# Optimization experiments

Measured on AMD Instinct MI355X. Metric: run time of the kernel, lower is better.

## Reference

```python
import jax, jax.numpy as jnp
import numpy as np
import math

# B graphs of exactly NMAX nodes each
N, B, NMAX, E = 131072, 256, 512, 1048576
F_IN, C, H, HEADS, NUM_CLASSES = 128, 32, 64, 4, 2
K1 = 128  # ceil(avg_num_nodes * pooling_ratio) = ceil(512 * 0.25)
SCALE = math.sqrt(H)  # GMT MAB scales by sqrt(dim_V), not sqrt(head_dim)


def gcn_conv(x, W, b, src, dst, n):
    h = x @ W
    deg = jax.ops.segment_sum(jnp.ones(dst.shape[0], x.dtype), dst, num_segments=n) + 1.0
    dinv = jax.lax.rsqrt(deg)
    msg = h[src] * (dinv[src] * dinv[dst])[:, None]
    out = jax.ops.segment_sum(msg, dst, num_segments=n)
    out = out + h * (dinv * dinv)[:, None]  # self-loop term
    return out + b


def mab(Qin, K, V, addmask, Wq, bq, Wo, bo):
    # GMT multihead attention block (layer_norm=False)
    Q = Qin @ Wq + bq
    b_, nq, _ = Q.shape
    dh = H // HEADS
    q = Q.reshape(b_, nq, HEADS, dh)
    k = K.reshape(b_, K.shape[1], HEADS, dh)
    v = V.reshape(b_, K.shape[1], HEADS, dh)
    s = jnp.einsum('bqhd,bkhd->bhqk', q, k) / SCALE
    if addmask is not None:
        s = s + addmask[:, None, None, :]  # mask invalid keys
    A = jax.nn.softmax(s, axis=-1)
    o = jnp.einsum('bhqk,bkhd->bqhd', A, v).reshape(b_, nq, H)
    o = Q + o
    return o + jax.nn.relu(o @ Wo + bo)


def _forward(x0, conv1_W, conv1_b, conv2_W, conv2_b, conv3_W, conv3_b,
             pool_lin1_W, pool_lin1_b,
             pma1_S, pma1_Wq, pma1_bq, pma1_Wk, pma1_bk, pma1_Wv, pma1_bv, pma1_Wo, pma1_bo,
             sab_Wq, sab_bq, sab_Wk, sab_bk, sab_Wv, sab_bv, sab_Wo, sab_bo,
             pma2_S, pma2_Wq, pma2_bq, pma2_Wk, pma2_bk, pma2_Wv, pma2_bv, pma2_Wo, pma2_bo,
             pool_lin2_W, pool_lin2_b, lin1_W, lin1_b, lin2_W, lin2_b,
             edge_index, batch):
    src, dst = edge_index[0], edge_index[1]
    x1 = jax.nn.relu(gcn_conv(x0, conv1_W, conv1_b, src, dst, N))
    x2 = jax.nn.relu(gcn_conv(x1, conv2_W, conv2_b, src, dst, N))
    x3 = jax.nn.relu(gcn_conv(x2, conv3_W, conv3_b, src, dst, N))
    xc = jnp.concatenate([x1, x2, x3], axis=-1)         # [N, 96]
    xl = xc @ pool_lin1_W + pool_lin1_b                 # [N, H] (GMT lin1)

    # to_dense_batch bookkeeping (batch is sorted per graph)
    counts = jax.ops.segment_sum(jnp.ones(N, jnp.int32), batch, num_segments=B)
    starts = jnp.cumsum(counts) - counts
    pos = jnp.arange(N, dtype=jnp.int32) - starts[batch]
    valid = jnp.zeros((B, NMAX), bool).at[batch, pos].set(True)
    addmask = jnp.where(valid, 0.0, -1e9).astype(xl.dtype)

    def dense(h):
        return jnp.zeros((B, NMAX, h.shape[-1]), h.dtype).at[batch, pos].set(h)

    # GMPool_G: seed queries attend over GCNConv-transformed node features
    Kd = dense(gcn_conv(xl, pma1_Wk, pma1_bk, src, dst, N))
    Vd = dense(gcn_conv(xl, pma1_Wv, pma1_bv, src, dst, N))
    Q = jnp.broadcast_to(pma1_S[None], (B, K1, H))
    bx = mab(Q, Kd, Vd, addmask, pma1_Wq, pma1_bq, pma1_Wo, pma1_bo)

    # SelfAtt (mask=None after first pool)
    bx = mab(bx, bx @ sab_Wk + sab_bk, bx @ sab_Wv + sab_bv, None,
             sab_Wq, sab_bq, sab_Wo, sab_bo)

    # GMPool_I with single seed (last pool -> 1 output node per graph)
    Q2 = jnp.broadcast_to(pma2_S[None], (B, 1, H))
    bx = mab(Q2, bx @ pma2_Wk + pma2_bk, bx @ pma2_Wv + pma2_bv, None,
             pma2_Wq, pma2_bq, pma2_Wo, pma2_bo)

    g = bx[:, 0] @ pool_lin2_W + pool_lin2_b            # [B, 32] (GMT lin2)
    h1 = jax.nn.relu(g @ lin1_W + lin1_b)               # dropout identity in eval
    logits = h1 @ lin2_W + lin2_b
    return jax.nn.log_softmax(logits, axis=-1)


def setup_inputs() -> dict:
    key = jax.random.key(0)
    ks = iter(jax.random.split(key, 80))
    def Wm(fi, fo):
        return jax.random.normal(next(ks), (fi, fo), jnp.float32) / np.sqrt(fi)
    def bv(fo):
        return jax.random.normal(next(ks), (fo,), jnp.float32) * 0.01
    inp = {}
    inp['x0'] = jax.random.normal(next(ks), (N, F_IN), jnp.float32)
    g = jax.random.randint(next(ks), (E,), 0, B)
    so = jax.random.randint(next(ks), (E,), 0, NMAX)
    do = jax.random.randint(next(ks), (E,), 0, NMAX)
    inp['edge_index'] = jnp.stack([g * NMAX + so, g * NMAX + do]).astype(jnp.int32)
    inp['batch'] = jnp.arange(N, dtype=jnp.int32) // NMAX
    inp['conv1_W'], inp['conv1_b'] = Wm(F_IN, C), bv(C)
    inp['conv2_W'], inp['conv2_b'] = Wm(C, C), bv(C)
    inp['conv3_W'], inp['conv3_b'] = Wm(C, C), bv(C)
    inp['pool_lin1_W'], inp['pool_lin1_b'] = Wm(3 * C, H), bv(H)
    inp['pma1_S'] = jax.random.normal(next(ks), (K1, H), jnp.float32)
    for p in ['pma1', 'sab', 'pma2']:
        for nm in ['q', 'k', 'v', 'o']:
            inp[p + '_W' + nm], inp[p + '_b' + nm] = Wm(H, H), bv(H)
    inp['pma2_S'] = jax.random.normal(next(ks), (1, H), jnp.float32)
    inp['pool_lin2_W'], inp['pool_lin2_b'] = Wm(H, C), bv(C)
    inp['lin1_W'], inp['lin1_b'] = Wm(C, 16), bv(16)
    inp['lin2_W'], inp['lin2_b'] = Wm(16, NUM_CLASSES), bv(NUM_CLASSES)
    return inp


def reference(x0, edge_index, batch, conv1_W, conv1_b, conv2_W, conv2_b, conv3_W, conv3_b,
              pool_lin1_W, pool_lin1_b,
              pma1_S, pma1_Wq, pma1_bq, pma1_Wk, pma1_bk, pma1_Wv, pma1_bv, pma1_Wo, pma1_bo,
              sab_Wq, sab_bq, sab_Wk, sab_bk, sab_Wv, sab_bv, sab_Wo, sab_bo,
              pma2_S, pma2_Wq, pma2_bq, pma2_Wk, pma2_bk, pma2_Wv, pma2_bv, pma2_Wo, pma2_bo,
              pool_lin2_W, pool_lin2_b, lin1_W, lin1_b, lin2_W, lin2_b):
    return _forward(x0, conv1_W, conv1_b, conv2_W, conv2_b, conv3_W, conv3_b,
                    pool_lin1_W, pool_lin1_b,
                    pma1_S, pma1_Wq, pma1_bq, pma1_Wk, pma1_bk, pma1_Wv, pma1_bv, pma1_Wo, pma1_bo,
                    sab_Wq, sab_bq, sab_Wk, sab_bk, sab_Wv, sab_bv, sab_Wo, sab_bo,
                    pma2_S, pma2_Wq, pma2_bq, pma2_Wk, pma2_bk, pma2_Wv, pma2_bv, pma2_Wo, pma2_bo,
                    pool_lin2_W, pool_lin2_b, lin1_W, lin1_b, lin2_W, lin2_b,
                    edge_index, batch)
```

## Files before the change

kernel.cpp:

```cpp
#include <hip/hip_runtime.h>
#include <hip/hip_bf16.h>

#define N_NODES 131072
#define NGRAPH  256
#define NMAXN   512
#define NEDGE   1048576
#define FIN     128
#define HDIM    64
#define K1Q     128
#define EPB     1024
#define NBLK    (NEDGE / EPB)

__global__ __launch_bounds__(256) void k_hist2(const int* __restrict__ dst,
                                               int* __restrict__ h) {
    __shared__ int lh[NGRAPH];
    const int tid = threadIdx.x;
    lh[tid] = 0;
    __syncthreads();
    const int base = blockIdx.x * EPB;
#pragma unroll
    for (int j = 0; j < 4; ++j)
        atomicAdd(&lh[dst[base + j * 256 + tid] >> 9], 1);
    __syncthreads();
    h[blockIdx.x * 256 + tid] = lh[tid];
}

__global__ __launch_bounds__(256) void k_scan_bins(int* __restrict__ h,
                                                   int* __restrict__ binTot) {
    const int b = blockIdx.x;
    const int tid = threadIdx.x;
    int v[4], s = 0;
#pragma unroll
    for (int j = 0; j < 4; ++j) { v[j] = h[(tid * 4 + j) * 256 + b]; s += v[j]; }
    __shared__ int sc[256];
    sc[tid] = s;
    __syncthreads();
    for (int o = 1; o < 256; o <<= 1) {
        int t = (tid >= o) ? sc[tid - o] : 0;
        __syncthreads();
        sc[tid] += t;
        __syncthreads();
    }
    int run = sc[tid] - s;
#pragma unroll
    for (int j = 0; j < 4; ++j) { int t = v[j]; h[(tid * 4 + j) * 256 + b] = run; run += t; }
    if (tid == 255) binTot[b] = sc[255];
}

__global__ __launch_bounds__(256) void k_binstart(const int* __restrict__ binTot,
                                                  int* __restrict__ starts) {
    const int tid = threadIdx.x;
    int v = binTot[tid];
    __shared__ int sc[256];
    sc[tid] = v;
    __syncthreads();
    for (int o = 1; o < 256; o <<= 1) {
        int t = (tid >= o) ? sc[tid - o] : 0;
        __syncthreads();
        sc[tid] += t;
        __syncthreads();
    }
    starts[tid] = sc[tid] - v;
    if (tid == 255) starts[256] = sc[255];
}

__global__ __launch_bounds__(256) void k_scatter2(const int* __restrict__ src,
                                                  const int* __restrict__ dst,
                                                  const int* __restrict__ h,
                                                  const int* __restrict__ starts,
                                                  int* __restrict__ epack) {
    __shared__ int base[NGRAPH];
    const int tid = threadIdx.x;
    base[tid] = h[blockIdx.x * 256 + tid] + starts[tid];
    __syncthreads();
    const int b0 = blockIdx.x * EPB;
#pragma unroll
    for (int j = 0; j < 4; ++j) {
        int e = b0 + j * 256 + tid;
        int d = dst[e];
        int pos = atomicAdd(&base[d >> 9], 1);
        epack[pos] = ((src[e] & (NMAXN - 1)) << 9) | (d & (NMAXN - 1));
    }
}

__global__ __launch_bounds__(256) void k_sort_dst(
    const int* __restrict__ epack, const int* __restrict__ starts,
    int* __restrict__ esrc, int* __restrict__ rowptr)
{
    __shared__ int hist[NMAXN];
    __shared__ int excl[NMAXN];
    __shared__ int psc[256];
    const int g = blockIdx.x, tid = threadIdx.x;
    const int e0 = starts[g], e1 = starts[g + 1];
    hist[tid] = 0; hist[tid + 256] = 0;
    __syncthreads();
    for (int e = e0 + tid; e < e1; e += 256)
        atomicAdd(&hist[epack[e] & (NMAXN - 1)], 1);
    __syncthreads();
    int a = hist[2 * tid], b = hist[2 * tid + 1];
    psc[tid] = a + b;
    __syncthreads();
    for (int o = 1; o < 256; o <<= 1) {
        int t = (tid >= o) ? psc[tid - o] : 0;
        __syncthreads();
        psc[tid] += t;
        __syncthreads();
    }
    int ep = psc[tid] - a - b;
    excl[2 * tid] = ep;
    excl[2 * tid + 1] = ep + a;
    __syncthreads();
    rowptr[g * NMAXN + 2 * tid]     = e0 + excl[2 * tid];
    rowptr[g * NMAXN + 2 * tid + 1] = e0 + excl[2 * tid + 1];
    if (g == NGRAPH - 1 && tid == 0) rowptr[N_NODES] = NEDGE;
    __syncthreads();
    for (int e = e0 + tid; e < e1; e += 256) {
        int p = epack[e];
        int d = p & (NMAXN - 1);
        int pos = e0 + atomicAdd(&excl[d], 1);
        esrc[pos] = p >> 9;
    }
}

__global__ void k_dinv2(const int* __restrict__ rowptr, float* __restrict__ d) {
    int i = blockIdx.x * blockDim.x + threadIdx.x;
    if (i < N_NODES) d[i] = rsqrtf((float)(rowptr[i + 1] - rowptr[i]) + 1.0f);
}

template<int TM, int K, int CO, int MODE>
__global__ __launch_bounds__(256) void k_gemm(
    const float* __restrict__ A, int lda,
    const float* __restrict__ W, const float* __restrict__ bias,
    float* __restrict__ out, int ldo, int M)
{
    constexpr int WTS = K + 4;
    __shared__ float As[TM * K];
    __shared__ float Wt[CO * WTS];
    const int tid = threadIdx.x;
    const int row0 = blockIdx.x * TM;

    for (int i = tid; i < K * CO; i += 256) {
        int k = i / CO, c = i - k * CO;
        Wt[c * WTS + k] = W[i];
    }
    constexpr int VR = K / 4;
    for (int i = tid; i < TM * VR; i += 256) {
        int r = i / VR, v = i - r * VR;
        int gr = row0 + r;
        float4 val = make_float4(0.f, 0.f, 0.f, 0.f);
        if (gr < M) val = *(const float4*)(A + (size_t)gr * lda + v * 4);
        *(float4*)(As + r * K + v * 4) = val;
    }
    __syncthreads();

    constexpr int G = 256 / CO;
    constexpr int RPT = TM / G;
    const int co = tid % CO;
    const int g = tid / CO;

    float acc[RPT];
#pragma unroll
    for (int r = 0; r < RPT; ++r) acc[r] = 0.f;

    const float* wrow = Wt + co * WTS;
    for (int kk = 0; kk < K / 4; ++kk) {
        float4 w = *(const float4*)(wrow + kk * 4);
#pragma unroll
        for (int r = 0; r < RPT; ++r) {
            float4 a = *(const float4*)(As + (g * RPT + r) * K + kk * 4);
            acc[r] += a.x * w.x + a.y * w.y + a.z * w.z + a.w * w.w;
        }
    }
    float b = 0.f;
    if (MODE >= 1) b = bias[co];
#pragma unroll
    for (int r = 0; r < RPT; ++r) {
        int gr = row0 + g * RPT + r;
        if (gr < M) {
            float v = acc[r] + b;
            if (MODE == 2) v = fmaxf(v, 0.f);
            out[(size_t)gr * ldo + co] = v;
        }
    }
}

template<int K, int RELU>
__global__ __launch_bounds__(256) void k_gcn_fused(
    const float* __restrict__ A, int lda,
    const float* __restrict__ W, int ldw,
    const float* __restrict__ bias,
    const float* __restrict__ dinv,
    const int* __restrict__ esrc, const int* __restrict__ rowptr,
    float* __restrict__ out, int ldo)
{
    constexpr int C   = 8192 / K;
    constexpr int NCH = NMAXN / C;
    constexpr int RPT = C / 8;
    constexpr int LS  = 36;
    constexpr int WTS = K + 4;
    __shared__ float U[NMAXN * LS];
    __shared__ float dl[NMAXN];
    float* As = U;
    float* Wt = U + 8192;
    const int g = blockIdx.x, tid = threadIdx.x;
    const int node0 = g * NMAXN;

    for (int i = tid; i < 32 * K; i += 256) {
        int k = i >> 5, co = i & 31;
        Wt[co * WTS + k] = W[k * ldw + co];
    }
    for (int i = tid; i < NMAXN; i += 256) dl[i] = dinv[node0 + i];

    const int co = tid & 31, grp = tid >> 5;
    float acc[64];
#pragma unroll
    for (int r = 0; r < 64; ++r) acc[r] = 0.f;

#pragma unroll
    for (int ch = 0; ch < NCH; ++ch) {
        __syncthreads();
        for (int i = tid; i < C * (K / 4); i += 256) {
            int r = i / (K / 4), v = i % (K / 4);
            *(float4*)(As + r * K + v * 4) =
                *(const float4*)(A + (size_t)(node0 + ch * C + r) * lda + v * 4);
        }
        __syncthreads();
        for (int kk = 0; kk < K / 4; ++kk) {
            float4 w = *(const float4*)(Wt + co * WTS + kk * 4);
#pragma unroll
            for (int r = 0; r < RPT; ++r) {
                float4 a = *(const float4*)(As + (grp * RPT + r) * K + kk * 4);
                acc[ch * RPT + r] += a.x * w.x + a.y * w.y + a.z * w.z + a.w * w.w;
            }
        }
    }
    __syncthreads();
    float* Tl = U;
#pragma unroll
    for (int ch = 0; ch < NCH; ++ch)
#pragma unroll
        for (int r = 0; r < RPT; ++r) {
            int row = ch * C + grp * RPT + r;
            Tl[row * LS + co] = acc[ch * RPT + r] * dl[row];
        }
    __syncthreads();
    for (int i = tid; i < NMAXN * 8; i += 256) {
        int n = i >> 3, c4 = (i & 7) << 2;
        float4 s = *(const float4*)(Tl + n * LS + c4);
        const int eb = rowptr[node0 + n], ee = rowptr[node0 + n + 1];
        for (int e = eb; e < ee; ++e) {
            const float4 v = *(const float4*)(Tl + esrc[e] * LS + c4);
            s.x += v.x; s.y += v.y; s.z += v.z; s.w += v.w;
        }
        float wv = dl[n];
        float4 b4 = *(const float4*)(bias + c4);
        float4 o;
        o.x = b4.x + wv * s.x; o.y = b4.y + wv * s.y;
        o.z = b4.z + wv * s.z; o.w = b4.w + wv * s.w;
        if (RELU) {
            o.x = fmaxf(o.x, 0.f); o.y = fmaxf(o.y, 0.f);
            o.z = fmaxf(o.z, 0.f); o.w = fmaxf(o.w, 0.f);
        }
        *(float4*)(out + (size_t)(node0 + n) * ldo + c4) = o;
    }
}

template<int NK, bool QSH>
__global__ __launch_bounds__(256) void k_attn(
    const float* __restrict__ Q, const float* __restrict__ K,
    const float* __restrict__ V, float* __restrict__ O)
{
    constexpr int KQ  = NK / 4;
    constexpr int MLF = 3 * 128 * 18;
    __shared__ float Ks[NK * 16];
    __shared__ float Vs[NK * 16];
    __shared__ float Mlsep[(NK * 16 >= MLF) ? 4 : MLF];
    float* Ml = (NK * 16 >= MLF) ? Ks : Mlsep;
    const int g = blockIdx.x >> 2;
    const int h = blockIdx.x & 3;
    const int tid = threadIdx.x;
    for (int i = tid; i < NK * 4; i += 256) {
        int k = i >> 2, dc = (i & 3) << 2;
        const size_t off = ((size_t)g * NK + k) * HDIM + h * 16 + dc;
        *(float4*)(Ks + k * 16 + dc) = *(const float4*)(K + off);
        *(float4*)(Vs + k * 16 + dc) = *(const float4*)(V + off);
    }
    __syncthreads();
    const int qs = tid & 63;
    const int quarter = tid >> 6;
    const int k0 = quarter * KQ;
    const float* qp0 = QSH ? (Q + (size_t)qs * HDIM + h * 16)
                           : (Q + ((size_t)g * K1Q + qs) * HDIM + h * 16);
    const float* qp1 = qp0 + 64 * HDIM;
    float qv0[16], qv1[16];
#pragma unroll
    for (int d = 0; d < 16; ++d) { qv0[d] = qp0[d]; qv1[d] = qp1[d]; }

    float m0 = -1e30f, l0 = 0.f, m1 = -1e30f, l1 = 0.f;
    float acc0[16], acc1[16];
#pragma unroll
    for (int d = 0; d < 16; ++d) { acc0[d] = 0.f; acc1[d] = 0.f; }

    for (int kt = 0; kt < KQ; kt += 8) {
        const int kb = k0 + kt;
        float s0[8], s1[8];
#pragma unroll
        for (int j = 0; j < 8; ++j) {
            float t0 = 0.f, t1 = 0.f;
#pragma unroll
            for (int d4 = 0; d4 < 4; ++d4) {
                float4 kv = *(const float4*)(Ks + (kb + j) * 16 + d4 * 4);
                t0 += qv0[d4*4] * kv.x + qv0[d4*4+1] * kv.y
                    + qv0[d4*4+2] * kv.z + qv0[d4*4+3] * kv.w;
                t1 += qv1[d4*4] * kv.x + qv1[d4*4+1] * kv.y
                    + qv1[d4*4+2] * kv.z + qv1[d4*4+3] * kv.w;
            }
            s0[j] = t0 * 0.125f; s1[j] = t1 * 0.125f;
        }
        float tm0 = fmaxf(fmaxf(fmaxf(s0[0], s0[1]), fmaxf(s0[2], s0[3])),
                          fmaxf(fmaxf(s0[4], s0[5]), fmaxf(s0[6], s0[7])));
        float tm1 = fmaxf(fmaxf(fmaxf(s1[0], s1[1]), fmaxf(s1[2], s1[3])),
                          fmaxf(fmaxf(s1[4], s1[5]), fmaxf(s1[6], s1[7])));
        if (tm0 > m0 + 8.f) {
            float cr = __expf(m0 - tm0);
            l0 *= cr;
#pragma unroll
            for (int d = 0; d < 16; ++d) acc0[d] *= cr;
            m0 = tm0;
        }
        if (tm1 > m1 + 8.f) {
            float cr = __expf(m1 - tm1);
            l1 *= cr;
#pragma unroll
            for (int d = 0; d < 16; ++d) acc1[d] *= cr;
            m1 = tm1;
        }
        float p0[8], p1[8];
#pragma unroll
        for (int j = 0; j < 8; ++j) {
            p0[j] = __expf(s0[j] - m0); l0 += p0[j];
            p1[j] = __expf(s1[j] - m1); l1 += p1[j];
        }
#pragma unroll
        for (int d4 = 0; d4 < 4; ++d4) {
#pragma unroll
            for (int j = 0; j < 8; ++j) {
                float4 v = *(const float4*)(Vs + (kb + j) * 16 + d4 * 4);
                acc0[d4*4]   += p0[j] * v.x;  acc1[d4*4]   += p1[j] * v.x;
                acc0[d4*4+1] += p0[j] * v.y;  acc1[d4*4+1] += p1[j] * v.y;
                acc0[d4*4+2] += p0[j] * v.z;  acc1[d4*4+2] += p1[j] * v.z;
                acc0[d4*4+3] += p0[j] * v.w;  acc1[d4*4+3] += p1[j] * v.w;
            }
        }
    }
    __syncthreads();
    if (quarter) {
        float* w0 = Ml + ((quarter - 1) * 128 + qs) * 18;
        float* w1 = Ml + ((quarter - 1) * 128 + qs + 64) * 18;
        w0[0] = m0; w0[1] = l0;
        w1[0] = m1; w1[1] = l1;
#pragma unroll
        for (int d = 0; d < 16; ++d) { w0[2 + d] = acc0[d]; w1[2 + d] = acc1[d]; }
    }
    __syncthreads();
    if (quarter == 0) {
#pragma unroll
        for (int qq = 0; qq < 2; ++qq) {
            const int q = qs + qq * 64;
            float m = qq ? m1 : m0, l = qq ? l1 : l0;
            float ac[16];
#pragma unroll
            for (int d = 0; d < 16; ++d) ac[d] = qq ? acc1[d] : acc0[d];
            float M = m;
#pragma unroll
            for (int p = 0; p < 3; ++p) M = fmaxf(M, Ml[(p * 128 + q) * 18]);
            float c = __expf(m - M);
            float L = l * c;
#pragma unroll
            for (int d = 0; d < 16; ++d) ac[d] *= c;
#pragma unroll
            for (int p = 0; p < 3; ++p) {
                const float* r = Ml + (p * 128 + q) * 18;
                float cp = __expf(r[0] - M);
                L += r[1] * cp;
#pragma unroll
                for (int d = 0; d < 16; ++d) ac[d] += r[2 + d] * cp;
            }
            float inv = 1.f / L;
            float* op = O + ((size_t)g * K1Q + q) * HDIM + h * 16;
#pragma unroll
            for (int d = 0; d < 16; ++d) op[d] = ac[d] * inv;
        }
    }
}

__global__ __launch_bounds__(256) void k_attn_pma2(
    const float* __restrict__ Q2p, const float* __restrict__ K3,
    const float* __restrict__ V3, float* __restrict__ O3)
{
    const int t = threadIdx.x;
    const int lane = t & 63;
    const int g = blockIdx.x * 4 + (t >> 6);
    const float q = Q2p[lane];
    const float* Kg = K3 + (size_t)g * 128 * HDIM + lane;
    const float* Vg = V3 + (size_t)g * 128 * HDIM + lane;
    float m = -1e30f, l = 0.f, acc = 0.f;
    for (int k = 0; k < 128; ++k) {
        float s = q * Kg[(size_t)k * HDIM];
        s += __shfl_xor(s, 1); s += __shfl_xor(s, 2);
        s += __shfl_xor(s, 4); s += __shfl_xor(s, 8);
        s *= 0.125f;
        float mn = fmaxf(m, s);
        float cr = __expf(m - mn), p = __expf(s - mn);
        l = l * cr + p;
        acc = acc * cr + p * Vg[(size_t)k * HDIM];
        m = mn;
    }
    O3[(size_t)g * HDIM + lane] = acc / l;
}

template<int NQ>
__global__ __launch_bounds__(256) void k_mab_epi(
    const float* __restrict__ AO, const float* __restrict__ Qsrc,
    const float* __restrict__ W, const float* __restrict__ bias,
    float* __restrict__ out, int M)
{
    constexpr int TM = 128, KK = 64, CO = 64, WTS = KK + 4;
    __shared__ float Os[TM * KK];
    __shared__ float Wt[CO * WTS];
    const int tid = threadIdx.x;
    const int row0 = blockIdx.x * TM;
    for (int i = tid; i < KK * CO; i += 256) {
        int k = i >> 6, c = i & 63;
        Wt[c * WTS + k] = W[i];
    }
    for (int i = tid; i < TM * 16; i += 256) {
        int r = i >> 4, v = (i & 15) << 2;
        int gr = row0 + r;
        float4 a = make_float4(0.f, 0.f, 0.f, 0.f);
        if (gr < M) {
            float4 x = *(const float4*)(AO + (size_t)gr * KK + v);
            int qr = (NQ == 0) ? gr : (NQ == 1 ? 0 : (gr & (NQ - 1)));
            float4 qv = *(const float4*)(Qsrc + (size_t)qr * KK + v);
            a.x = x.x + qv.x; a.y = x.y + qv.y; a.z = x.z + qv.z; a.w = x.w + qv.w;
        }
        *(float4*)(Os + r * KK + v) = a;
    }
    __syncthreads();
    const int co = tid & 63, g = tid >> 6;
    float acc[32];
#pragma unroll
    for (int r = 0; r < 32; ++r) acc[r] = 0.f;
    const float* wrow = Wt + co * WTS;
    for (int kk = 0; kk < KK / 4; ++kk) {
        float4 w = *(const float4*)(wrow + kk * 4);
#pragma unroll
        for (int r = 0; r < 32; ++r) {
            float4 a = *(const float4*)(Os + (g * 32 + r) * KK + kk * 4);
            acc[r] += a.x * w.x + a.y * w.y + a.z * w.z + a.w * w.w;
        }
    }
    float b = bias[co];
#pragma unroll
    for (int r = 0; r < 32; ++r) {
        int gr = row0 + g * 32 + r;
        if (gr < M) {
            float o = Os[(g * 32 + r) * KK + co];
            out[(size_t)gr * CO + co] = o + fmaxf(acc[r] + b, 0.f);
        }
    }
}

__global__ __launch_bounds__(64) void k_head(
    const float* __restrict__ BX3,
    const float* __restrict__ W1, const float* __restrict__ b1,
    const float* __restrict__ W2, const float* __restrict__ b2,
    const float* __restrict__ W3, const float* __restrict__ b3,
    float* __restrict__ outp)
{
    __shared__ float w1[64 * 32], w2[32 * 16], w3[32], bb1[32], bb2[16], bb3[2];
    const int tid = threadIdx.x;
    for (int i = tid; i < 64 * 32; i += 64) w1[i] = W1[i];
    for (int i = tid; i < 32 * 16; i += 64) w2[i] = W2[i];
    if (tid < 32) { w3[tid] = W3[tid]; bb1[tid] = b1[tid]; }
    if (tid < 16) bb2[tid] = b2[tid];
    if (tid < 2)  bb3[tid] = b3[tid];
    __syncthreads();
    const int g = blockIdx.x * 64 + tid;
    float x[64];
#pragma unroll
    for (int v = 0; v < 16; ++v) {
        float4 t = *(const float4*)(BX3 + (size_t)g * 64 + v * 4);
        x[v*4] = t.x; x[v*4+1] = t.y; x[v*4+2] = t.z; x[v*4+3] = t.w;
    }
    float gv[32];
    for (int c = 0; c < 32; ++c) {
        float a = bb1[c];
        for (int k = 0; k < 64; ++k) a += x[k] * w1[k * 32 + c];
        gv[c] = a;
    }
    float h1[16];
    for (int c = 0; c < 16; ++c) {
        float a = bb2[c];
        for (int k = 0; k < 32; ++k) a += gv[k] * w2[k * 16 + c];
        h1[c] = fmaxf(a, 0.f);
    }
    float z0 = bb3[0], z1 = bb3[1];
    for (int k = 0; k < 16; ++k) { z0 += h1[k] * w3[k * 2]; z1 += h1[k] * w3[k * 2 + 1]; }
    float mm = fmaxf(z0, z1);
    float ls = mm + logf(__expf(z0 - mm) + __expf(z1 - mm));
    outp[g * 2]     = z0 - ls;
    outp[g * 2 + 1] = z1 - ls;
}

extern "C" void kernel_launch(void* const* d_in, const int* in_sizes, int n_in,
                              void* d_out, int out_size, void* d_ws, size_t ws_size,
                              hipStream_t stream) {
    const float* x0  = (const float*)d_in[0];
    const int*   ei  = (const int*)d_in[1];
    const float* c1W = (const float*)d_in[3];  const float* c1b = (const float*)d_in[4];
    const float* c2W = (const float*)d_in[5];  const float* c2b = (const float*)d_in[6];
    const float* c3W = (const float*)d_in[7];  const float* c3b = (const float*)d_in[8];
    const float* plW = (const float*)d_in[9];  const float* plb = (const float*)d_in[10];
    const float* S1  = (const float*)d_in[11];
    const float* p1Wq = (const float*)d_in[12]; const float* p1bq = (const float*)d_in[13];
    const float* p1Wk = (const float*)d_in[14]; const float* p1bk = (const float*)d_in[15];
    const float* p1Wv = (const float*)d_in[16]; const float* p1bv = (const float*)d_in[17];
    const float* p1Wo = (const float*)d_in[18]; const float* p1bo = (const float*)d_in[19];
    const float* sWq  = (const float*)d_in[20]; const float* sbq  = (const float*)d_in[21];
    const float* sWk  = (const float*)d_in[22]; const float* sbk  = (const float*)d_in[23];
    const float* sWv  = (const float*)d_in[24]; const float* sbv  = (const float*)d_in[25];
    const float* sWo  = (const float*)d_in[26]; const float* sbo  = (const float*)d_in[27];
    const float* p2Wq = (const float*)d_in[28]; const float* p2bq = (const float*)d_in[29];
    const float* p2Wk = (const float*)d_in[30]; const float* p2bk = (const float*)d_in[31];
    const float* p2Wv = (const float*)d_in[32]; const float* p2bv = (const float*)d_in[33];
    const float* p2Wo = (const float*)d_in[34]; const float* p2bo = (const float*)d_in[35];
    const float* S2   = (const float*)d_in[36];
    const float* pl2W = (const float*)d_in[37]; const float* pl2b = (const float*)d_in[38];
    const float* l1W  = (const float*)d_in[39]; const float* l1b  = (const float*)d_in[40];
    const float* l2W  = (const float*)d_in[41]; const float* l2b  = (const float*)d_in[42];

    const int* src = ei;
    const int* dst = ei + NEDGE;

    float* ws = (float*)d_ws;
    float* dinv = ws;
    size_t off = N_NODES;
    int* epack  = (int*)(ws + off); off += NEDGE;
    int* h      = (int*)(ws + off); off += NBLK * 256;
    int* binTot = (int*)(ws + off); off += 256;
    int* starts = (int*)(ws + off); off += 257;
    int* esrc   = (int*)(ws + off); off += NEDGE;
    int* rowptr = (int*)(ws + off); off += N_NODES + 1;
    off = (off + 255) & ~(size_t)255;
    float* Qp  = ws + off; off += K1Q * HDIM;
    float* Q2p = ws + off; off += HDIM;
    float* O3  = ws + off; off += NGRAPH * HDIM;
    float* BX3 = ws + off; off += NGRAPH * HDIM;
    off = (off + 1023) & ~(size_t)1023;
    float* P0 = ws + off;
    const size_t SL = (size_t)N_NODES * 32;
    float* XC  = P0 + 2 * SL;
    float* XL  = P0 + 5 * SL;
    float* KD  = P0;
    float* VD  = P0 + 2 * SL;
    float* O1  = P0 + 4 * SL;
    float* BX1 = P0 + 4 * SL + SL / 2;
    float* Qs  = P0;
    float* Ks_ = P0 + SL / 2;
    float* Vs_ = P0 + SL;
    float* O2  = P0 + SL + SL / 2;
    float* BX2 = P0 + 2 * SL;
    float* K3  = P0 + 2 * SL + SL / 2;
    float* V3  = P0 + 3 * SL;

    k_hist2<<<NBLK, 256, 0, stream>>>(dst, h);
    k_scan_bins<<<256, 256, 0, stream>>>(h, binTot);
    k_binstart<<<1, 256, 0, stream>>>(binTot, starts);
    k_scatter2<<<NBLK, 256, 0, stream>>>(src, dst, h, starts, epack);
    k_sort_dst<<<NGRAPH, 256, 0, stream>>>(epack, starts, esrc, rowptr);
    k_dinv2<<<512, 256, 0, stream>>>(rowptr, dinv);

    k_gcn_fused<128, 1><<<NGRAPH, 256, 0, stream>>>(x0, FIN, c1W, 32, c1b, dinv, esrc, rowptr, XC, 96);
    k_gcn_fused<32, 1><<<NGRAPH, 256, 0, stream>>>(XC, 96, c2W, 32, c2b, dinv, esrc, rowptr, XC + 32, 96);
    k_gcn_fused<32, 1><<<NGRAPH, 256, 0, stream>>>(XC + 32, 96, c3W, 32, c3b, dinv, esrc, rowptr, XC + 64, 96);

    k_gemm<64, 96, 64, 1><<<2048, 256, 0, stream>>>(XC, 96, plW, plb, XL, 64, N_NODES);

    k_gcn_fused<64, 0><<<NGRAPH, 256, 0, stream>>>(XL, 64, p1Wk, 64, p1bk, dinv, esrc, rowptr, KD, 64);
    k_gcn_fused<64, 0><<<NGRAPH, 256, 0, stream>>>(XL, 64, p1Wk + 32, 64, p1bk + 32, dinv, esrc, rowptr, KD + 32, 64);
    k_gcn_fused<64, 0><<<NGRAPH, 256, 0, stream>>>(XL, 64, p1Wv, 64, p1bv, dinv, esrc, rowptr, VD, 64);
    k_gcn_fused<64, 0><<<NGRAPH, 256, 0, stream>>>(XL, 64, p1Wv + 32, 64, p1bv + 32, dinv, esrc, rowptr, VD + 32, 64);

    k_gemm<128, 64, 64, 1><<<1, 256, 0, stream>>>(S1, 64, p1Wq, p1bq, Qp, 64, K1Q);
    k_attn<512, true><<<NGRAPH * 4, 256, 0, stream>>>(Qp, KD, VD, O1);
    k_mab_epi<128><<<256, 256, 0, stream>>>(O1, Qp, p1Wo, p1bo, BX1, NGRAPH * K1Q);

    k_gemm<128, 64, 64, 1><<<256, 256, 0, stream>>>(BX1, 64, sWq, sbq, Qs, 64, NGRAPH * K1Q);
    k_gemm<128, 64, 64, 1><<<256, 256, 0, stream>>>(BX1, 64, sWk, sbk, Ks_, 64, NGRAPH * K1Q);
    k_gemm<128, 64, 64, 1><<<256, 256, 0, stream>>>(BX1, 64, sWv, sbv, Vs_, 64, NGRAPH * K1Q);
    k_attn<128, false><<<NGRAPH * 4, 256, 0, stream>>>(Qs, Ks_, Vs_, O2);
    k_mab_epi<0><<<256, 256, 0, stream>>>(O2, Qs, sWo, sbo, BX2, NGRAPH * K1Q);

    k_gemm<128, 64, 64, 1><<<256, 256, 0, stream>>>(BX2, 64, p2Wk, p2bk, K3, 64, NGRAPH * K1Q);
    k_gemm<128, 64, 64, 1><<<256, 256, 0, stream>>>(BX2, 64, p2Wv, p2bv, V3, 64, NGRAPH * K1Q);
    k_gemm<128, 64, 64, 1><<<1, 256, 0, stream>>>(S2, 64, p2Wq, p2bq, Q2p, 64, 1);
    k_attn_pma2<<<64, 256, 0, stream>>>(Q2p, K3, V3, O3);
    k_mab_epi<1><<<2, 256, 0, stream>>>(O3, Q2p, p2Wo, p2bo, BX3, NGRAPH);

    k_head<<<4, 64, 0, stream>>>(BX3, pl2W, pl2b, l1W, l1b, l2W, l2b,
                                 (float*)d_out);
}
```

Baseline: 1.339 ms.

## Split fused per-graph GCN kernels into wide GEMM plus separate aggregation

Each fused GCN kernel did both the dense transform and the neighbour aggregation inside one block per graph, so only 256 blocks ran. The transform now goes through the generic k_gemm with 1024-2048 blocks and writes to a temporary buffer. A new aggregation kernel then loads that buffer, scales it by dinv, sums over neighbours in shared memory and adds bias and ReLU. The goal is to spread the matmul across many more blocks and use fewer registers per thread, at the cost of an extra global write and read of the intermediate features. The K and V output buffers are relocated so they do not collide with the temporary.

Measured after the change: 1.170 ms. 1.14x faster.

```diff
diff --git a/kernel.cpp b/kernel.cpp
--- a/kernel.cpp
+++ b/kernel.cpp
@@ -184,79 +184,44 @@
     }
 }
 
-template<int K, int RELU>
-__global__ __launch_bounds__(256) void k_gcn_fused(
-    const float* __restrict__ A, int lda,
-    const float* __restrict__ W, int ldw,
-    const float* __restrict__ bias,
-    const float* __restrict__ dinv,
+template<int RELU>
+__global__ __launch_bounds__(256) void k_gcn_agg2(
+    const float* __restrict__ T, int ldt,
+    const float* __restrict__ dinv, const float* __restrict__ bias,
     const int* __restrict__ esrc, const int* __restrict__ rowptr,
     float* __restrict__ out, int ldo)
 {
-    constexpr int C   = 8192 / K;
-    constexpr int NCH = NMAXN / C;
-    constexpr int RPT = C / 8;
-    constexpr int LS  = 36;
-    constexpr int WTS = K + 4;
-    __shared__ float U[NMAXN * LS];
+    constexpr int LS = 36;
+    __shared__ float Tl[NMAXN * LS];
     __shared__ float dl[NMAXN];
-    float* As = U;
-    float* Wt = U + 8192;
-    const int g = blockIdx.x, tid = threadIdx.x;
+    const int g = blockIdx.x;
+    const int tid = threadIdx.x;
     const int node0 = g * NMAXN;
 
-    for (int i = tid; i < 32 * K; i += 256) {
-        int k = i >> 5, co = i & 31;
-        Wt[co * WTS + k] = W[k * ldw + co];
-    }
     for (int i = tid; i < NMAXN; i += 256) dl[i] = dinv[node0 + i];
-
-    const int co = tid & 31, grp = tid >> 5;
-    float acc[64];
-#pragma unroll
-    for (int r = 0; r < 64; ++r) acc[r] = 0.f;
-
-#pragma unroll
-    for (int ch = 0; ch < NCH; ++ch) {
-        __syncthreads();
-        for (int i = tid; i < C * (K / 4); i += 256) {
-            int r = i / (K / 4), v = i % (K / 4);
-            *(float4*)(As + r * K + v * 4) =
-                *(const float4*)(A + (size_t)(node0 + ch * C + r) * lda + v * 4);
-        }
-        __syncthreads();
-        for (int kk = 0; kk < K / 4; ++kk) {
-            float4 w = *(const float4*)(Wt + co * WTS + kk * 4);
-#pragma unroll
-            for (int r = 0; r < RPT; ++r) {
-                float4 a = *(const float4*)(As + (grp * RPT + r) * K + kk * 4);
-                acc[ch * RPT + r] += a.x * w.x + a.y * w.y + a.z * w.z + a.w * w.w;
-            }
-        }
-    }
-    __syncthreads();
-    float* Tl = U;
-#pragma unroll
-    for (int ch = 0; ch < NCH; ++ch)
-#pragma unroll
-        for (int r = 0; r < RPT; ++r) {
-            int row = ch * C + grp * RPT + r;
-            Tl[row * LS + co] = acc[ch * RPT + r] * dl[row];
-        }
+    __syncthreads();
+    for (int i = tid; i < NMAXN * 8; i += 256) {
+        int r = i >> 3, c4 = (i & 7) << 2;
+        float4 v = *(const float4*)(T + (size_t)(node0 + r) * ldt + c4);
+        float w = dl[r];
+        v.x *= w; v.y *= w; v.z *= w; v.w *= w;
+        *(float4*)(Tl + r * LS + c4) = v;
+    }
     __syncthreads();
     for (int i = tid; i < NMAXN * 8; i += 256) {
         int n = i >> 3, c4 = (i & 7) << 2;
-        float4 s = *(const float4*)(Tl + n * LS + c4);
+        float4 acc = *(const float4*)(Tl + n * LS + c4);
         const int eb = rowptr[node0 + n], ee = rowptr[node0 + n + 1];
         for (int e = eb; e < ee; ++e) {
-            const float4 v = *(const float4*)(Tl + esrc[e] * LS + c4);
-            s.x += v.x; s.y += v.y; s.z += v.z; s.w += v.w;
-        }
-        float wv = dl[n];
+            int ls = esrc[e];
+            const float4 v = *(const float4*)(Tl + ls * LS + c4);
+            acc.x += v.x; acc.y += v.y; acc.z += v.z; acc.w += v.w;
+        }
+        float w = dl[n];
         float4 b4 = *(const float4*)(bias + c4);
         float4 o;
-        o.x = b4.x + wv * s.x; o.y = b4.y + wv * s.y;
-        o.z = b4.z + wv * s.z; o.w = b4.w + wv * s.w;
+        o.x = b4.x + w * acc.x; o.y = b4.y + w * acc.y;
+        o.z = b4.z + w * acc.z; o.w = b4.w + w * acc.w;
         if (RELU) {
             o.x = fmaxf(o.x, 0.f); o.y = fmaxf(o.y, 0.f);
             o.z = fmaxf(o.z, 0.f); o.w = fmaxf(o.w, 0.f);
@@ -560,10 +525,12 @@
     off = (off + 1023) & ~(size_t)1023;
     float* P0 = ws + off;
     const size_t SL = (size_t)N_NODES * 32;
+    float* T32 = P0;
+    float* T64 = P0;
     float* XC  = P0 + 2 * SL;
     float* XL  = P0 + 5 * SL;
-    float* KD  = P0;
-    float* VD  = P0 + 2 * SL;
+    float* KD  = P0 + 2 * SL;
+    float* VD  = P0 + 5 * SL;
     float* O1  = P0 + 4 * SL;
     float* BX1 = P0 + 4 * SL + SL / 2;
     float* Qs  = P0;
@@ -581,16 +548,21 @@
     k_sort_dst<<<NGRAPH, 256, 0, stream>>>(epack, starts, esrc, rowptr);
     k_dinv2<<<512, 256, 0, stream>>>(rowptr, dinv);
 
-    k_gcn_fused<128, 1><<<NGRAPH, 256, 0, stream>>>(x0, FIN, c1W, 32, c1b, dinv, esrc, rowptr, XC, 96);
-    k_gcn_fused<32, 1><<<NGRAPH, 256, 0, stream>>>(XC, 96, c2W, 32, c2b, dinv, esrc, rowptr, XC + 32, 96);
-    k_gcn_fused<32, 1><<<NGRAPH, 256, 0, stream>>>(XC + 32, 96, c3W, 32, c3b, dinv, esrc, rowptr, XC + 64, 96);
+    k_gemm<64, 128, 32, 0><<<2048, 256, 0, stream>>>(x0, FIN, c1W, nullptr, T32, 32, N_NODES);
+    k_gcn_agg2<1><<<256, 256, 0, stream>>>(T32, 32, dinv, c1b, esrc, rowptr, XC, 96);
+    k_gemm<128, 32, 32, 0><<<1024, 256, 0, stream>>>(XC, 96, c2W, nullptr, T32, 32, N_NODES);
+    k_gcn_agg2<1><<<256, 256, 0, stream>>>(T32, 32, dinv, c2b, esrc, rowptr, XC + 32, 96);
+    k_gemm<128, 32, 32, 0><<<1024, 256, 0, stream>>>(XC + 32, 96, c3W, nullptr, T32, 32, N_NODES);
+    k_gcn_agg2<1><<<256, 256, 0, stream>>>(T32, 32, dinv, c3b, esrc, rowptr, XC + 64, 96);
 
     k_gemm<64, 96, 64, 1><<<2048, 256, 0, stream>>>(XC, 96, plW, plb, XL, 64, N_NODES);
 
-    k_gcn_fused<64, 0><<<NGRAPH, 256, 0, stream>>>(XL, 64, p1Wk, 64, p1bk, dinv, esrc, rowptr, KD, 64);
-    k_gcn_fused<64, 0><<<NGRAPH, 256, 0, stream>>>(XL, 64, p1Wk + 32, 64, p1bk + 32, dinv, esrc, rowptr, KD + 32, 64);
-    k_gcn_fused<64, 0><<<NGRAPH, 256, 0, stream>>>(XL, 64, p1Wv, 64, p1bv, dinv, esrc, rowptr, VD, 64);
-    k_gcn_fused<64, 0><<<NGRAPH, 256, 0, stream>>>(XL, 64, p1Wv + 32, 64, p1bv + 32, dinv, esrc, rowptr, VD + 32, 64);
+    k_gemm<128, 64, 64, 0><<<1024, 256, 0, stream>>>(XL, 64, p1Wk, nullptr, T64, 64, N_NODES);
+    k_gcn_agg2<0><<<256, 256, 0, stream>>>(T64, 64, dinv, p1bk, esrc, rowptr, KD, 64);
+    k_gcn_agg2<0><<<256, 256, 0, stream>>>(T64 + 32, 64, dinv, p1bk + 32, esrc, rowptr, KD + 32, 64);
+    k_gemm<128, 64, 64, 0><<<1024, 256, 0, stream>>>(XL, 64, p1Wv, nullptr, T64, 64, N_NODES);
+    k_gcn_agg2<0><<<256, 256, 0, stream>>>(T64, 64, dinv, p1bv, esrc, rowptr, VD, 64);
+    k_gcn_agg2<0><<<256, 256, 0, stream>>>(T64 + 32, 64, dinv, p1bv + 32, esrc, rowptr, VD + 32, 64);
 
     k_gemm<128, 64, 64, 1><<<1, 256, 0, stream>>>(S1, 64, p1Wq, p1bq, Qp, 64, K1Q);
     k_attn<512, true><<<NGRAPH * 4, 256, 0, stream>>>(Qp, KD, VD, O1);
```
